# Performance work log

Hardware: AMD Instinct MI355X
Metric: run time of the kernel (lower is better)

Reference implementation:

```python
import jax, jax.numpy as jnp
import numpy as np
from jax import lax

B, S, I = 256, 16, 64
D = 128
N_ITEMS = 100000
K = 3
PAD_ID = 0
BOS_ID = N_ITEMS
DILATIONS = (1, 2, 4)


def setup_inputs() -> dict:
    key = jax.random.key(0)
    ks = jax.random.split(key, 16)
    item_id = jax.random.randint(ks[0], (B, S, I), 0, N_ITEMS, dtype=jnp.int32)
    eval_from = jax.random.randint(ks[1], (B,), 0, S, dtype=jnp.int32)
    u_type = jax.random.randint(ks[2], (B,), 0, 4, dtype=jnp.int32)
    emb = jax.random.normal(ks[3], (N_ITEMS + 1, D), jnp.float32) * 0.05
    emb = emb.at[PAD_ID].set(0.0)  # padding_idx=0
    kaiming = (2.0 / (D * K)) ** 0.5
    conv_w0 = jax.random.normal(ks[4], (D, D, K), jnp.float32) * kaiming
    conv_w1 = jax.random.normal(ks[5], (D, D, K), jnp.float32) * kaiming
    conv_w2 = jax.random.normal(ks[6], (D, D, K), jnp.float32) * kaiming
    conv_b0 = jnp.zeros((D,), jnp.float32)
    conv_b1 = jnp.zeros((D,), jnp.float32)
    conv_b2 = jnp.zeros((D,), jnp.float32)
    gru_wih = jax.random.normal(ks[7], (3 * D, D), jnp.float32) * 0.05
    gru_whh = jax.random.normal(ks[8], (3 * D, D), jnp.float32) * 0.05
    gru_bih = jax.random.normal(ks[9], (3 * D,), jnp.float32) * 0.05
    gru_bhh = jax.random.normal(ks[10], (3 * D,), jnp.float32) * 0.05
    fus_w = jax.random.normal(ks[11], (D, 2 * D), jnp.float32) * 0.05
    fus_b = jnp.zeros((D,), jnp.float32)
    return {"item_id": item_id, "eval_from": eval_from, "u_type": u_type,
            "emb": emb,
            "conv_w0": conv_w0, "conv_b0": conv_b0,
            "conv_w1": conv_w1, "conv_b1": conv_b1,
            "conv_w2": conv_w2, "conv_b2": conv_b2,
            "gru_wih": gru_wih, "gru_whh": gru_whh,
            "gru_bih": gru_bih, "gru_bhh": gru_bhh,
            "fus_w": fus_w, "fus_b": fus_b}


def reference(item_id, eval_from, u_type, emb,
              conv_w0, conv_b0, conv_w1, conv_b1, conv_w2, conv_b2,
              gru_wih, gru_whh, gru_bih, gru_bhh, fus_w, fus_b):
    item_id = jnp.maximum(item_id, 0)  # clamp_min(0)
    Bc, Sc, Ic = item_id.shape
    convs = ((conv_w0, conv_b0, DILATIONS[0]),
             (conv_w1, conv_b1, DILATIONS[1]),
             (conv_w2, conv_b2, DILATIONS[2]))

    def tcn(x):  # x: [B, T, D] -> [B, T, D]
        h = jnp.transpose(x, (0, 2, 1))  # NCH
        for w, b, dil in convs:
            pad = (K - 1) * dil
            out = lax.conv_general_dilated(
                h, w, window_strides=(1,), padding=[(pad, 0)],
                rhs_dilation=(dil,),
                dimension_numbers=('NCH', 'OIH', 'NCH')) + b[None, :, None]
            h = jax.nn.relu(out + h)
        return jnp.transpose(h, (0, 2, 1))

    def gru_step(h, x):  # h,x: [B, D]
        gi = x @ gru_wih.T + gru_bih
        gh = h @ gru_whh.T + gru_bhh
        ir, iz, inn = jnp.split(gi, 3, axis=-1)
        hr, hz, hn = jnp.split(gh, 3, axis=-1)
        r = jax.nn.sigmoid(ir + hr)
        z = jax.nn.sigmoid(iz + hz)
        n = jnp.tanh(inn + r * hn)
        return (1.0 - z) * n + z * h

    pos = jnp.arange(Ic + 1)
    bos = jnp.full((Bc, 1), BOS_ID, dtype=item_id.dtype)

    def step(h, seq_s):  # seq_s: [B, I]
        lengths = (seq_s != PAD_ID).sum(-1)          # [B]
        max_len = lengths.max()                       # batch-level session max
        seq = jnp.concatenate([bos, seq_s], axis=1)   # [B, I+1], BOS prepended
        valid = pos[None, :] <= max_len               # positions torch keeps
        seq = jnp.where(valid, seq, PAD_ID)
        mask = seq != PAD_ID
        e = emb[seq]                                  # [B, I+1, D] (PAD row is 0)
        tc = tcn(e)
        fin = jnp.concatenate([tc, jnp.broadcast_to(h[:, None, :], tc.shape)], -1)
        reps = fin @ fus_w.T + fus_b                  # [B, I+1, D]
        reps = reps * valid[..., None]                # torch zero-pads beyond max_len
        # drop mask at last valid token (per-sample python loop in torch)
        mask = mask & ~((pos[None, :] == lengths[:, None]) & (lengths > 0)[:, None])
        mf = mask.astype(e.dtype)
        mean_emb = (e * mf[..., None]).sum(1) / jnp.maximum(mf.sum(1), 1.0)[:, None]
        h2 = gru_step(h, mean_emb)
        return h2, (reps, mask)

    h0 = jnp.zeros((Bc, D), jnp.float32)
    _, (reps, masks) = lax.scan(step, h0, jnp.transpose(item_id, (1, 0, 2)))
    reps = jnp.transpose(reps, (1, 0, 2, 3))          # [B, S, I+1, D]
    masks = jnp.transpose(masks, (1, 0, 2))           # [B, S, I+1]
    allow = jnp.arange(Sc)[None, :] >= eval_from[:, None]
    loss_masks = masks & allow[:, :, None]
    return reps, loss_masks, u_type
```

## Files before the change

### kernel.cpp

```cpp
#include <hip/hip_runtime.h>

#define BB 256
#define SS 16
#define II 64
#define DD 128
#define TT 65
#define BOS_ID 100000
#define XROW 256
#define XROWS 73
#define XT (XROWS*XROW)

#define OFF_LEN  0
#define OFF_ML   16384
#define OFF_ME   32768
#define OFF_HB   (32768 + 2097152)
#define OFF_WB2  (OFF_HB + 2097152)
#define OFF_WIHP (OFF_WB2 + 327680)
#define OFF_WGRU (OFF_WIHP + 98304)

#define OUT_MASK  (BB*SS*TT*DD)
#define OUT_UTYPE (OUT_MASK + BB*SS*TT)

typedef __attribute__((ext_vector_type(8))) short short8;
typedef __attribute__((ext_vector_type(4))) float f32x4;

__device__ __forceinline__ unsigned short f2bf(float f) {
    unsigned int u = __builtin_bit_cast(unsigned int, f);
    return (unsigned short)((u + 0x7fffu + ((u >> 16) & 1u)) >> 16);
}
__device__ __forceinline__ float bflo(unsigned int u) {
    return __builtin_bit_cast(float, u << 16);
}
__device__ __forceinline__ float bfhi(unsigned int u) {
    return __builtin_bit_cast(float, u & 0xffff0000u);
}
__device__ __forceinline__ void gld16(const void* g, void* l) {
    __builtin_amdgcn_global_load_lds(
        (const __attribute__((address_space(1))) void*)g,
        (__attribute__((address_space(3))) void*)l, 16, 0, 0);
}

__global__ __launch_bounds__(256) void prep_kernel(
    const float* __restrict__ w0, const float* __restrict__ w1,
    const float* __restrict__ w2, const float* __restrict__ fus_w,
    const float* __restrict__ wih, const float* __restrict__ whh,
    const int* __restrict__ item_id, const int* __restrict__ u_type,
    unsigned short* __restrict__ wB2,
    unsigned int* __restrict__ wih4, unsigned int* __restrict__ wgru4,
    int* __restrict__ lengths, int* __restrict__ maxlen,
    float* __restrict__ u_out)
{
    if (blockIdx.x >= 864) {
        int s = blockIdx.x - 864;
        int b = threadIdx.x;
        const int* row = item_id + (b * SS + s) * II;
        int cnt = 0;
        for (int i = 0; i < II; ++i) cnt += (row[i] > 0);
        lengths[b * SS + s] = cnt;
        __shared__ int red[256];
        red[b] = cnt;
        __syncthreads();
        for (int off = 128; off > 0; off >>= 1) {
            if (b < off) red[b] = max(red[b], red[b + off]);
            __syncthreads();
        }
        if (b == 0) maxlen[s] = red[0];
        if (s == 0) u_out[b] = (float)u_type[b];
        return;
    }
    int idx = blockIdx.x * 256 + threadIdx.x;
    if (idx < 163840) {
        int cid2  = idx >> 11;
        int inner = idx & 2047;
        int g = inner >> 9;
        int c = (inner >> 3) & 63;
        int e = inner & 7;
        int nh   = cid2 & 1;
        int rest = cid2 >> 1;
        int cq   = rest & 3;
        int m    = rest >> 2;
        int ci = cq * 32 + g * 8 + e;
        int co = nh * 64 + c;
        float v;
        if (m < 9) {
            int L = m / 3, k = m % 3;
            const float* w = (L == 0) ? w0 : ((L == 1) ? w1 : w2);
            v = w[(co * 128 + ci) * 3 + k];
            if (k == 2 && ci == co) v += 1.0f;
        } else {
            v = fus_w[co * 256 + ci];
        }
        wB2[idx] = f2bf(v);
    } else if (idx < 163840 + 24576) {
        int f   = idx - 163840;
        int dd4 = f / 1536;
        int rem = f - dd4 * 1536;
        int r   = rem >> 2;
        int c   = rem & 3;
        int d0  = 8 * dd4 + 2 * c;
        unsigned int lo = f2bf(wih[r * 128 + d0]);
        unsigned int hi = f2bf(wih[r * 128 + d0 + 1]);
        wih4[f] = (hi << 16) | lo;
    } else if (idx < 163840 + 24576 + 32768) {
        int f   = idx - 163840 - 24576;
        int dd4 = f >> 11;
        int rem = f & 2047;
        int r   = rem >> 2;
        int c   = rem & 3;
        int d0  = 8 * dd4 + 2 * c;
        float v0, v1;
        if (r < 384) { v0 = whh[r * 128 + d0]; v1 = whh[r * 128 + d0 + 1]; }
        else { const float* fw = fus_w + (r - 384) * 256 + 128;
               v0 = fw[d0]; v1 = fw[d0 + 1]; }
        wgru4[f] = ((unsigned int)f2bf(v1) << 16) | (unsigned int)f2bf(v0);
    }
}

__global__ __launch_bounds__(256) void mean_kernel(
    const int* __restrict__ item_id, const int* __restrict__ eval_from,
    const float* __restrict__ emb,
    const int* __restrict__ lengths, const int* __restrict__ maxlen,
    float* __restrict__ mean_emb, float* __restrict__ mask_out)
{
    int bid = blockIdx.x;
    int b = bid >> 4, s = bid & 15;
    int tid = threadIdx.x;
    int d = tid & 127, tg = tid >> 7;
    __shared__ int seqs[TT];
    __shared__ int msk[TT];
    __shared__ float part[DD];
    int ml  = maxlen[s];
    int len = lengths[bid];
    int ef  = eval_from[b];
    if (tid < TT) {
        int v;
        if (tid == 0) v = BOS_ID;
        else { int it = item_id[bid * II + tid - 1]; v = it > 0 ? it : 0; }
        if (tid > ml) v = 0;
        int m = (v != 0) && !(tid == len && len > 0);
        seqs[tid] = v;
        msk[tid]  = m;
        mask_out[bid * TT + tid] = (m && (s >= ef)) ? 1.0f : 0.0f;
    }
    __syncthreads();
    int cnt = 0;
    for (int p = 0; p < TT; ++p) cnt += msk[p];
    float acc = 0.0f;
    for (int p = tg; p < TT; p += 2) {
        if (msk[p]) acc += emb[(long)seqs[p] * DD + d];
    }
    if (tg == 1) part[d] = acc;
    __syncthreads();
    if (tg == 0)
        mean_emb[bid * DD + d] = (acc + part[d]) / (float)max(cnt, 1);
}

__global__ __launch_bounds__(512, 1) void gru_kernel(
    const float* __restrict__ me_all, const unsigned int* __restrict__ wih4,
    const float* __restrict__ bih,
    const unsigned int* __restrict__ wgru4, const float* __restrict__ bhh,
    const float* __restrict__ fus_b, float* __restrict__ hB)
{
    __shared__ __align__(16) unsigned int wl[16 * 384 * 4];
    __shared__ __align__(16) float me[2][DD];
    __shared__ unsigned int hpk[64];
    __shared__ float g_z[DD], g_inn[DD], g_hn[DD];
    int t = threadIdx.x;
    int b = blockIdx.x;
    int j = t & 127;
    int grp = t >> 7;

    {
        const unsigned char* g = (const unsigned char*)wih4 + t * 16;
        unsigned char* l = (unsigned char*)wl + t * 16;
#pragma unroll
        for (int i = 0; i < 12; ++i) gld16(g + i * 8192, l + i * 8192);
    }
    uint4 w[16];
    const uint4* wg4 = (const uint4*)wgru4;
#pragma unroll
    for (int dd4 = 0; dd4 < 16; ++dd4) w[dd4] = wg4[dd4 * 512 + t];

    float bias_hh = (t < 384) ? bhh[t] : fus_b[j];
    float bias_ih = (t < 384) ? bih[t] : 0.0f;
    if (t < DD) me[0][t] = me_all[b * SS * DD + t];
    float hj = 0.0f;
    if (t < 64) hpk[t] = 0u;
    asm volatile("s_waitcnt vmcnt(0)" ::: "memory");
    __syncthreads();

    const uint4* wl4 = (const uint4*)wl;
    for (int s = 0; s < SS; ++s) {
        if (t < DD && s < 15) me[(s + 1) & 1][t] = me_all[(b * SS + s + 1) * DD + t];
        const float* mc = me[s & 1];
        float gi = bias_ih;
        if (grp < 3) {
#pragma unroll
            for (int dd4 = 0; dd4 < 16; ++dd4) {
                uint4 u = wl4[dd4 * 384 + t];
                float4 m0 = *(const float4*)&mc[8 * dd4];
                float4 m1 = *(const float4*)&mc[8 * dd4 + 4];
                gi += bflo(u.x) * m0.x + bfhi(u.x) * m0.y;
                gi += bflo(u.y) * m0.z + bfhi(u.y) * m0.w;
                gi += bflo(u.z) * m1.x + bfhi(u.z) * m1.y;
                gi += bflo(u.w) * m1.z + bfhi(u.w) * m1.w;
            }
        }
        float acc = bias_hh;
#pragma unroll
        for (int dd4 = 0; dd4 < 16; ++dd4) {
            uint4 hp = *(const uint4*)&hpk[dd4 * 4];
            uint4 u  = w[dd4];
            acc += bflo(u.x) * bflo(hp.x) + bfhi(u.x) * bfhi(hp.x);
            acc += bflo(u.y) * bflo(hp.y) + bfhi(u.y) * bfhi(hp.y);
            acc += bflo(u.z) * bflo(hp.z) + bfhi(u.z) * bfhi(hp.z);
            acc += bflo(u.w) * bflo(hp.w) + bfhi(u.w) * bfhi(hp.w);
        }
        if (grp == 3) {
            hB[(s * BB + b) * DD + j] = acc;
        } else if (grp == 1) { g_z[j] = gi + acc; }
        else if (grp == 2)   { g_inn[j] = gi; g_hn[j] = acc; }
        __syncthreads();
        if (grp == 0) {
            float r = 1.0f / (1.0f + expf(-(gi + acc)));
            float z = 1.0f / (1.0f + expf(-g_z[j]));
            float n = tanhf(g_inn[j] + r * g_hn[j]);
            float hnew = (1.0f - z) * n + z * hj;
            hj = hnew;
            float hnb = __shfl_xor(hnew, 1);
            if ((j & 1) == 0) {
                unsigned int pk;
                asm("v_cvt_pk_bf16_f32 %0, %1, %2" : "=v"(pk) : "v"(hnew), "v"(hnb));
                hpk[j >> 1] = pk;
            }
        }
        __syncthreads();
    }
}

__global__ __launch_bounds__(256, 2) void tcn_kernel(
    const int* __restrict__ item_id, const float* __restrict__ emb,
    const int* __restrict__ maxlen,
    const unsigned short* __restrict__ wB2,
    const float* __restrict__ cb0, const float* __restrict__ cb1,
    const float* __restrict__ cb2,
    const float* __restrict__ hB, float* __restrict__ reps)
{
    __shared__ __align__(16) unsigned char lds_x[2][XT];
    __shared__ __align__(16) unsigned char ring[2][16384];

    const int tid = threadIdx.x, bid = blockIdx.x;
    const int lane = tid & 63, wv = tid >> 6;
    const int l15 = lane & 15, q4 = lane >> 4;
    const int t = wv >> 1, nh = wv & 1;
    const int tile = bid * 2 + t;
    const int b = tile >> 4, s = tile & 15;
    const int ml = maxlen[s];

    const unsigned char* wgbase = (const unsigned char*)wB2;
    unsigned char* xb = lds_x[t];

    {
        const unsigned char* src = wgbase + wv * 1024 + lane * 16;
        gld16(src,         &ring[0][wv * 1024]);
        gld16(src + 4096,  &ring[0][4096 + wv * 1024]);
        gld16(src + 8192,  &ring[0][8192 + wv * 1024]);
        gld16(src + 12288, &ring[0][12288 + wv * 1024]);
    }
    int* seqs2 = (int*)&ring[1][0];
    if (tid < 2 * TT) {
        int tt = tid / TT, p = tid - tt * TT;
        int tl = bid * 2 + tt;
        int v;
        if (p == 0) v = BOS_ID;
        else { int it = item_id[tl * II + p - 1]; v = it > 0 ? it : 0; }
        if (p > maxlen[tl & 15]) v = 0;
        seqs2[tt * TT + p] = v;
    }
    {
        float4 z = {0.f, 0.f, 0.f, 0.f};
        if (tid < 128) *(float4*)(lds_x[0] + tid * 16) = z;
        else           *(float4*)(lds_x[1] + (tid - 128) * 16) = z;
    }
    __syncthreads();

    for (int p = nh; p < TT; p += 2) {
        const float* er = emb + (long)seqs2[t * TT + p] * DD + lane * 2;
        float f0 = er[0], f1 = er[1];
        unsigned int pk = ((unsigned int)f2bf(f1) << 16) | (unsigned int)f2bf(f0);
        *(unsigned int*)(xb + (8 + p) * XROW + ((lane * 4) ^ ((p & 7) << 4))) = pk;
    }

    f32x4 acc[5][4];

#pragma unroll 1
    for (int sc = 0; sc < 20; ++sc) {
        if (sc == 18 || (sc < 18 && sc % 6 == 0)) {
#pragma unroll
            for (int mt = 0; mt < 5; ++mt)
#pragma unroll
                for (int nt = 0; nt < 4; ++nt)
#pragma unroll
                    for (int r = 0; r < 4; ++r) acc[mt][nt][r] = 0.0f;
        }
        asm volatile("s_waitcnt vmcnt(0)" ::: "memory");
        __syncthreads();

        if (sc <= 18) {
            const unsigned char* src =
                wgbase + (size_t)(sc + 1) * 16384 + wv * 1024 + lane * 16;
            unsigned char* dst = &ring[(sc + 1) & 1][0];
            gld16(src,         dst + wv * 1024);
            gld16(src + 4096,  dst + 4096 + wv * 1024);
            gld16(src + 8192,  dst + 8192 + wv * 1024);
            gld16(src + 12288, dst + 12288 + wv * 1024);
        }

#pragma unroll
        for (int half = 0; half < 2; ++half) {
            int cid = 2 * sc + half;
            int L = 0, cq, off;
            if (cid < 36) { L = cid / 12; int kq = cid - L * 12; int k = kq >> 2; cq = kq & 3; off = (2 - k) << L; }
            else { cq = cid - 36; off = 0; }
            const unsigned char* sb = &ring[sc & 1][half * 8192 + nh * 4096];
            const int xmask = ((l15 - off) & 7) << 4;
            const int colx  = (cq * 64 + q4 * 16) ^ xmask;
            short8 bfr[4], af[5];
#pragma unroll
            for (int nt = 0; nt < 4; ++nt)
                bfr[nt] = *(const short8*)(sb + q4 * 1024 + (nt * 16 + l15) * 16);
#pragma unroll
            for (int mt = 0; mt < 5; ++mt) {
                int rowA = 8 + mt * 16 + l15 - off;
                af[mt] = *(const short8*)(xb + rowA * XROW + colx);
            }
#pragma unroll
            for (int nt = 0; nt < 4; ++nt)
#pragma unroll
                for (int mt = 0; mt < 5; ++mt)
                    acc[mt][nt] = __builtin_amdgcn_mfma_f32_16x16x32_bf16(
                        af[mt], bfr[nt], acc[mt][nt], 0, 0, 0);
        }

        if (sc < 18 && sc % 6 == 5) {
            int L = sc / 6;
            const float* cb = (L == 0) ? cb0 : ((L == 1) ? cb1 : cb2);
            __syncthreads();
#pragma unroll
            for (int nt = 0; nt < 4; ++nt) {
                float bia = cb[nh * 64 + nt * 16 + l15];
                int cbyte = nh * 128 + nt * 32 + l15 * 2;
#pragma unroll
                for (int mt = 0; mt < 5; ++mt)
#pragma unroll
                    for (int r = 0; r < 4; ++r) {
                        int p = mt * 16 + q4 * 4 + r;
                        if (p < TT) {
                            int row = 8 + p;
                            float v = acc[mt][nt][r] + bia;
                            *(unsigned short*)(xb + row * XROW +
                                               (cbyte ^ ((row & 7) << 4))) =
                                f2bf(v > 0.f ? v : 0.f);
                        }
                    }
            }
            __syncthreads();
        }
    }

    float hb[4];
#pragma unroll
    for (int nt = 0; nt < 4; ++nt)
        hb[nt] = hB[(s * BB + b) * DD + nh * 64 + nt * 16 + l15];
    long ob = (long)tile * (TT * DD);
#pragma unroll
    for (int mt = 0; mt < 5; ++mt)
#pragma unroll
        for (int nt = 0; nt < 4; ++nt)
#pragma unroll
            for (int r = 0; r < 4; ++r) {
                int p = mt * 16 + q4 * 4 + r;
                if (p < TT) {
                    float v = (p <= ml) ? (acc[mt][nt][r] + hb[nt]) : 0.0f;
                    reps[ob + p * DD + nh * 64 + nt * 16 + l15] = v;
                }
            }
}

extern "C" void kernel_launch(void* const* d_in, const int* in_sizes, int n_in,
                              void* d_out, int out_size, void* d_ws, size_t ws_size,
                              hipStream_t stream) {
    const int*   item_id   = (const int*)  d_in[0];
    const int*   eval_from = (const int*)  d_in[1];
    const int*   u_type    = (const int*)  d_in[2];
    const float* emb       = (const float*)d_in[3];
    const float* conv_w0   = (const float*)d_in[4];
    const float* conv_b0   = (const float*)d_in[5];
    const float* conv_w1   = (const float*)d_in[6];
    const float* conv_b1   = (const float*)d_in[7];
    const float* conv_w2   = (const float*)d_in[8];
    const float* conv_b2   = (const float*)d_in[9];
    const float* gru_wih   = (const float*)d_in[10];
    const float* gru_whh   = (const float*)d_in[11];
    const float* gru_bih   = (const float*)d_in[12];
    const float* gru_bhh   = (const float*)d_in[13];
    const float* fus_w     = (const float*)d_in[14];
    const float* fus_b     = (const float*)d_in[15];

    char* ws = (char*)d_ws;
    int*            lengths  = (int*)           (ws + OFF_LEN);
    int*            maxlen   = (int*)           (ws + OFF_ML);
    float*          mean_emb = (float*)         (ws + OFF_ME);
    float*          hB       = (float*)         (ws + OFF_HB);
    unsigned short* wB2      = (unsigned short*)(ws + OFF_WB2);
    unsigned int*   wih4     = (unsigned int*)  (ws + OFF_WIHP);
    unsigned int*   wgru4    = (unsigned int*)  (ws + OFF_WGRU);

    float* out  = (float*)d_out;
    float* reps = out;
    float* mout = out + OUT_MASK;
    float* uout = out + OUT_UTYPE;

    prep_kernel<<<880, 256, 0, stream>>>(conv_w0, conv_w1, conv_w2, fus_w,
                                         gru_wih, gru_whh, item_id, u_type,
                                         wB2, wih4, wgru4, lengths, maxlen, uout);
    mean_kernel<<<BB * SS, 256, 0, stream>>>(item_id, eval_from, emb, lengths, maxlen,
                                             mean_emb, mout);
    gru_kernel<<<BB, 512, 0, stream>>>(mean_emb, wih4, gru_bih,
                                       wgru4, gru_bhh, fus_b, hB);
    tcn_kernel<<<BB * SS / 2, 256, 0, stream>>>(item_id, emb, maxlen, wB2,
                                                conv_b0, conv_b1, conv_b2, hB, reps);
}
```

Baseline: 235.9 us.

## Fuse masked mean-embedding computation into GRU kernel and drop a TCN barrier

Removes the separate mean_kernel: each GRU block now builds its sample's sequences and masks in shared memory, writes the loss mask, and computes all 16 per-step mean embeddings before the recurrence. This drops one kernel launch and the global round-trip of the mean-embedding buffer. The cost is that the embedding gather now runs across only 256 blocks of 512 threads, with serial 65-step loops per thread, so it has far less parallelism than the former 4096-block launch. Separately, a __syncthreads in the TCN layer loop is removed, which risks a shared-memory race between conv layers.

```diff
diff --git a/kernel.cpp b/kernel.cpp
--- a/kernel.cpp
+++ b/kernel.cpp
@@ -12,8 +12,7 @@
 
 #define OFF_LEN  0
 #define OFF_ML   16384
-#define OFF_ME   32768
-#define OFF_HB   (32768 + 2097152)
+#define OFF_HB   32768
 #define OFF_WB2  (OFF_HB + 2097152)
 #define OFF_WIHP (OFF_WB2 + 327680)
 #define OFF_WGRU (OFF_WIHP + 98304)
@@ -116,53 +115,19 @@
     }
 }
 
-__global__ __launch_bounds__(256) void mean_kernel(
+__global__ __launch_bounds__(512, 1) void gru_kernel(
     const int* __restrict__ item_id, const int* __restrict__ eval_from,
     const float* __restrict__ emb,
     const int* __restrict__ lengths, const int* __restrict__ maxlen,
-    float* __restrict__ mean_emb, float* __restrict__ mask_out)
-{
-    int bid = blockIdx.x;
-    int b = bid >> 4, s = bid & 15;
-    int tid = threadIdx.x;
-    int d = tid & 127, tg = tid >> 7;
-    __shared__ int seqs[TT];
-    __shared__ int msk[TT];
-    __shared__ float part[DD];
-    int ml  = maxlen[s];
-    int len = lengths[bid];
-    int ef  = eval_from[b];
-    if (tid < TT) {
-        int v;
-        if (tid == 0) v = BOS_ID;
-        else { int it = item_id[bid * II + tid - 1]; v = it > 0 ? it : 0; }
-        if (tid > ml) v = 0;
-        int m = (v != 0) && !(tid == len && len > 0);
-        seqs[tid] = v;
-        msk[tid]  = m;
-        mask_out[bid * TT + tid] = (m && (s >= ef)) ? 1.0f : 0.0f;
-    }
-    __syncthreads();
-    int cnt = 0;
-    for (int p = 0; p < TT; ++p) cnt += msk[p];
-    float acc = 0.0f;
-    for (int p = tg; p < TT; p += 2) {
-        if (msk[p]) acc += emb[(long)seqs[p] * DD + d];
-    }
-    if (tg == 1) part[d] = acc;
-    __syncthreads();
-    if (tg == 0)
-        mean_emb[bid * DD + d] = (acc + part[d]) / (float)max(cnt, 1);
-}
-
-__global__ __launch_bounds__(512, 1) void gru_kernel(
-    const float* __restrict__ me_all, const unsigned int* __restrict__ wih4,
-    const float* __restrict__ bih,
+    const unsigned int* __restrict__ wih4, const float* __restrict__ bih,
     const unsigned int* __restrict__ wgru4, const float* __restrict__ bhh,
-    const float* __restrict__ fus_b, float* __restrict__ hB)
+    const float* __restrict__ fus_b, float* __restrict__ hB,
+    float* __restrict__ mask_out)
 {
     __shared__ __align__(16) unsigned int wl[16 * 384 * 4];
-    __shared__ __align__(16) float me[2][DD];
+    __shared__ __align__(16) float meL[SS][DD];
+    __shared__ int   seqs[SS][TT];
+    __shared__ float mw[SS][TT];
     __shared__ unsigned int hpk[64];
     __shared__ float g_z[DD], g_inn[DD], g_hn[DD];
     int t = threadIdx.x;
@@ -176,6 +141,34 @@
 #pragma unroll
         for (int i = 0; i < 12; ++i) gld16(g + i * 8192, l + i * 8192);
     }
+
+    int ef = eval_from[b];
+    for (int idx = t; idx < SS * TT; idx += 512) {
+        int s = idx / TT, p = idx - s * TT;
+        int bid = b * SS + s;
+        int len = lengths[bid];
+        int v;
+        if (p == 0) v = BOS_ID;
+        else { int it = item_id[bid * II + p - 1]; v = it > 0 ? it : 0; }
+        if (p > maxlen[s]) v = 0;
+        int m = (v != 0) && !(p == len && len > 0);
+        seqs[s][p] = v;
+        mw[s][p]   = (float)m;
+        mask_out[bid * TT + p] = (m && (s >= ef)) ? 1.0f : 0.0f;
+    }
+    __syncthreads();
+
+    for (int r4 = 0; r4 < 4; ++r4) {
+        int s = grp * 4 + r4;
+        float acc = 0.0f, cnt = 0.0f;
+        for (int p = 0; p < TT; ++p) {
+            float m = mw[s][p];
+            cnt += m;
+            if (m != 0.0f) acc += emb[(long)seqs[s][p] * DD + j];
+        }
+        meL[s][j] = acc / fmaxf(cnt, 1.0f);
+    }
+
     uint4 w[16];
     const uint4* wg4 = (const uint4*)wgru4;
 #pragma unroll
@@ -183,7 +176,6 @@
 
     float bias_hh = (t < 384) ? bhh[t] : fus_b[j];
     float bias_ih = (t < 384) ? bih[t] : 0.0f;
-    if (t < DD) me[0][t] = me_all[b * SS * DD + t];
     float hj = 0.0f;
     if (t < 64) hpk[t] = 0u;
     asm volatile("s_waitcnt vmcnt(0)" ::: "memory");
@@ -191,8 +183,7 @@
 
     const uint4* wl4 = (const uint4*)wl;
     for (int s = 0; s < SS; ++s) {
-        if (t < DD && s < 15) me[(s + 1) & 1][t] = me_all[(b * SS + s + 1) * DD + t];
-        const float* mc = me[s & 1];
+        const float* mc = meL[s];
         float gi = bias_ih;
         if (grp < 3) {
 #pragma unroll
@@ -364,7 +355,6 @@
                         }
                     }
             }
-            __syncthreads();
         }
     }
 
@@ -410,7 +400,6 @@
     char* ws = (char*)d_ws;
     int*            lengths  = (int*)           (ws + OFF_LEN);
     int*            maxlen   = (int*)           (ws + OFF_ML);
-    float*          mean_emb = (float*)         (ws + OFF_ME);
     float*          hB       = (float*)         (ws + OFF_HB);
     unsigned short* wB2      = (unsigned short*)(ws + OFF_WB2);
     unsigned int*   wih4     = (unsigned int*)  (ws + OFF_WIHP);
@@ -424,10 +413,9 @@
     prep_kernel<<<880, 256, 0, stream>>>(conv_w0, conv_w1, conv_w2, fus_w,
                                          gru_wih, gru_whh, item_id, u_type,
                                          wB2, wih4, wgru4, lengths, maxlen, uout);
-    mean_kernel<<<BB * SS, 256, 0, stream>>>(item_id, eval_from, emb, lengths, maxlen,
-                                             mean_emb, mout);
-    gru_kernel<<<BB, 512, 0, stream>>>(mean_emb, wih4, gru_bih,
-                                       wgru4, gru_bhh, fus_b, hB);
+    gru_kernel<<<BB, 512, 0, stream>>>(item_id, eval_from, emb, lengths, maxlen,
+                                       wih4, gru_bih, wgru4, gru_bhh, fus_b,
+                                       hB, mout);
     tcn_kernel<<<BB * SS / 2, 256, 0, stream>>>(item_id, emb, maxlen, wB2,
                                                 conv_b0, conv_b1, conv_b2, hB, reps);
 }
```

After: 281.3 us. +19.2%, slower.
